# Kernel tuning notes

Hardware: AMD Instinct MI355X
Metric: run time of the kernel (lower is better)

The kernel has to match this reference:

```python
import jax, jax.numpy as jnp
import numpy as np

N = 100000       # nodes
E = 1600000      # edges (avg degree 16)
IN_DIM = 128
HIDDEN = 128


def _glorot(key, shape):
    s = 1.0 / np.sqrt(shape[0])
    return jax.random.uniform(key, shape, minval=-s, maxval=s, dtype=jnp.float32)


def setup_inputs() -> dict:
    key = jax.random.key(0)
    ks = jax.random.split(key, 8)
    x = jax.random.normal(ks[0], (N, IN_DIM), dtype=jnp.float32)
    edge_index = jax.random.randint(ks[1], (2, E), 0, N, dtype=jnp.int32)
    W0 = _glorot(ks[2], (IN_DIM, HIDDEN))
    b0 = jnp.zeros((HIDDEN,), dtype=jnp.float32)
    W1 = _glorot(ks[3], (HIDDEN, HIDDEN))
    b1 = jnp.zeros((HIDDEN,), dtype=jnp.float32)
    W2 = _glorot(ks[4], (HIDDEN, HIDDEN))
    b2 = jnp.zeros((HIDDEN,), dtype=jnp.float32)
    return {"x": x, "edge_index": edge_index,
            "W0": W0, "b0": b0, "W1": W1, "b1": b1, "W2": W2, "b2": b2}


def _gcn_conv(x, row, col, norm, W, b):
    # x' = W x, then out[i] = sum_{j in N(i) U {i}} norm_ji * x'[j], + bias
    h = x @ W                              # [N, out]
    msg = norm[:, None] * h[row]           # [E+N, out] gather + scale
    out = jax.ops.segment_sum(msg, col, num_segments=N)  # scatter-add
    return out + b


def reference(x, edge_index, W0, b0, W1, b1, W2, b2):
    # PyG GCNConv default: add self-loops, symmetric normalization D^-1/2 A D^-1/2
    self_loops = jnp.arange(N, dtype=edge_index.dtype)
    row = jnp.concatenate([edge_index[0], self_loops])  # sources
    col = jnp.concatenate([edge_index[1], self_loops])  # destinations
    deg = jax.ops.segment_sum(jnp.ones_like(col, dtype=x.dtype), col, num_segments=N)
    dinv = jax.lax.rsqrt(deg)              # deg >= 1 thanks to self-loops
    norm = dinv[row] * dinv[col]           # [E+N]

    h = _gcn_conv(x, row, col, norm, W0, b0)
    h = jax.nn.relu(h)                     # dropout: eval mode (identity)
    h = _gcn_conv(h, row, col, norm, W1, b1)
    h = jax.nn.relu(h)
    return _gcn_conv(h, row, col, norm, W2, b2)
```

## Files before the change

### kernel.cpp

```cpp
#include <hip/hip_runtime.h>

#define HID 128
#define BR  128
#define FILL_CHUNK 2048

typedef _Float16 f16;
typedef f16 f16x2 __attribute__((ext_vector_type(2)));
typedef f16 f16x4 __attribute__((ext_vector_type(4)));
typedef f16 f16x8 __attribute__((ext_vector_type(8)));
typedef float f32x4 __attribute__((ext_vector_type(4)));

static __device__ __forceinline__ float2 h2f(unsigned int u) {
    f16x2 v;
    __builtin_memcpy(&v, &u, 4);
    return make_float2((float)v[0], (float)v[1]);
}


__global__ void k_deg_count(const int* __restrict__ col, int* __restrict__ cnt, int E) {
    int e = blockIdx.x * 256 + threadIdx.x;
    if (e < E) atomicAdd(&cnt[col[e]], 1);
}

__global__ void k_scan_block(const int* __restrict__ cnt, int* __restrict__ excl,
                             int* __restrict__ bsum, float* __restrict__ dinv, int N) {
    __shared__ int s[256];
    int i = blockIdx.x * 256 + threadIdx.x;
    int v = (i < N) ? cnt[i] : 0;
    if (i < N) dinv[i] = 1.0f / sqrtf((float)(v + 1));
    s[threadIdx.x] = v;
    __syncthreads();
    for (int off = 1; off < 256; off <<= 1) {
        int t = (threadIdx.x >= off) ? s[threadIdx.x - off] : 0;
        __syncthreads();
        s[threadIdx.x] += t;
        __syncthreads();
    }
    if (i < N) excl[i] = s[threadIdx.x] - v;
    if (threadIdx.x == 255) bsum[blockIdx.x] = s[255];
}

__global__ __launch_bounds__(1024) void k_scan_bsum(int* __restrict__ bsum, int nb) {
    __shared__ int s[1024];
    int i = threadIdx.x;
    int v = (i < nb) ? bsum[i] : 0;
    s[i] = v;
    __syncthreads();
    for (int off = 1; off < 1024; off <<= 1) {
        int t = (i >= off) ? s[i - off] : 0;
        __syncthreads();
        s[i] += t;
        __syncthreads();
    }
    if (i < nb) bsum[i] = s[i] - v;
}

__global__ void k_scan_add(int* __restrict__ row_ptr, const int* __restrict__ bsum,
                           int* __restrict__ fill, int N, int E) {
    int i = blockIdx.x * 256 + threadIdx.x;
    if (i < N) {
        int v = row_ptr[i] + bsum[blockIdx.x];
        row_ptr[i] = v;
        fill[i] = v;
    }
    if (i == 0) row_ptr[N] = E;
}

__global__ void k_fill(const int* __restrict__ row, const int* __restrict__ col,
                       int* __restrict__ fill, int* __restrict__ csr_src, int E, int N) {
    const int xcd = blockIdx.x & 7;
    const int chunk = blockIdx.x >> 3;
    const int per = (N + 7) >> 3;
    const int lo = xcd * per;
    const int hi = min(N, lo + per);
    const int eend = min(E, (chunk + 1) * FILL_CHUNK);
    for (int e = chunk * FILL_CHUNK + threadIdx.x; e < eend; e += 256) {
        int c = col[e];
        if (c >= lo && c < hi) {
            int p = atomicAdd(&fill[c], 1);
            csr_src[p] = row[e];
        }
    }
}


__global__ void k_wprep(const float* __restrict__ W, f16* __restrict__ out) {
    int i = blockIdx.x * 256 + threadIdx.x;
    if (i >= 4096) return;
    int k = i >> 5, n0 = (i & 31) * 4;
    float4 v = reinterpret_cast<const float4*>(W)[i];
    float vv[4] = {v.x, v.y, v.z, v.w};
#pragma unroll
    for (int e = 0; e < 4; ++e) {
        int n = n0 + e;
        int idx = (k >> 3) * 1024 + n * 8 + (k & 7);
        f16 h = (f16)vv[e];
        out[idx] = h;
        out[16384 + idx] = (f16)(vv[e] - (float)h);
    }
}


__global__ __launch_bounds__(512, 4) void k_gemm(const float* __restrict__ X,
                                                 const f16* __restrict__ Wt,
                                                 const float* __restrict__ dinv,
                                                 f16* __restrict__ H,
                                                 int N, int relu_in) {
    __shared__ f16 Xs[2 * 16384];
    const int t = threadIdx.x;
    const int row0 = blockIdx.x * BR;

    const int w  = t >> 6;
    const int l  = t & 63;
    const int lg = l >> 4;
    const int li = l & 15;
    const int rg = w >> 2;
    const int cg = w & 3;

    f16x8 Bh[2][4], Bl[2][4];
#pragma unroll
    for (int cb = 0; cb < 2; ++cb) {
        const int ncol = cg * 32 + cb * 16 + li;
#pragma unroll
        for (int ks = 0; ks < 4; ++ks) {
            const int idx = (ks * 4 + lg) * 1024 + ncol * 8;
            Bh[cb][ks] = *reinterpret_cast<const f16x8*>(&Wt[idx]);
            Bl[cb][ks] = *reinterpret_cast<const f16x8*>(&Wt[16384 + idx]);
        }
    }

    for (int i = t; i < 4096; i += 512) {
        int r = i >> 5, q = i & 31;
        int gr = row0 + r;
        float4 v = make_float4(0.f, 0.f, 0.f, 0.f);
        if (gr < N) {
            v = reinterpret_cast<const float4*>(X + (size_t)gr * HID)[q];
            if (relu_in) {
                v.x = fmaxf(v.x, 0.f); v.y = fmaxf(v.y, 0.f);
                v.z = fmaxf(v.z, 0.f); v.w = fmaxf(v.w, 0.f);
            }
        }
        f16 h0 = (f16)v.x, h1 = (f16)v.y, h2 = (f16)v.z, h3 = (f16)v.w;
        f16 l0 = (f16)(v.x - (float)h0), l1 = (f16)(v.y - (float)h1);
        f16 l2 = (f16)(v.z - (float)h2), l3 = (f16)(v.w - (float)h3);
        int base = r * 128 + (((q >> 1) ^ (r & 7)) * 8) + (q & 1) * 4;
        *reinterpret_cast<f16x4*>(&Xs[base])         = (f16x4){h0, h1, h2, h3};
        *reinterpret_cast<f16x4*>(&Xs[16384 + base]) = (f16x4){l0, l1, l2, l3};
    }
    __syncthreads();

    f32x4 acc[4][2];
#pragma unroll
    for (int rb = 0; rb < 4; ++rb)
#pragma unroll
        for (int cb = 0; cb < 2; ++cb) acc[rb][cb] = (f32x4){0.f, 0.f, 0.f, 0.f};

#pragma unroll
    for (int rb = 0; rb < 4; ++rb) {
        const int arow = rg * 64 + rb * 16 + li;
#pragma unroll
        for (int ks = 0; ks < 4; ++ks) {
            const int idx = arow * 128 + (((ks * 4 + lg) ^ (arow & 7)) * 8);
            f16x8 Ah = *reinterpret_cast<const f16x8*>(&Xs[idx]);
            f16x8 Al = *reinterpret_cast<const f16x8*>(&Xs[16384 + idx]);
#pragma unroll
            for (int cb = 0; cb < 2; ++cb) {
                acc[rb][cb] = __builtin_amdgcn_mfma_f32_16x16x32_f16(Ah, Bh[cb][ks], acc[rb][cb], 0, 0, 0);
                acc[rb][cb] = __builtin_amdgcn_mfma_f32_16x16x32_f16(Ah, Bl[cb][ks], acc[rb][cb], 0, 0, 0);
                acc[rb][cb] = __builtin_amdgcn_mfma_f32_16x16x32_f16(Al, Bh[cb][ks], acc[rb][cb], 0, 0, 0);
            }
        }
    }

#pragma unroll
    for (int rb = 0; rb < 4; ++rb) {
#pragma unroll
        for (int r = 0; r < 4; ++r) {
            const int grow = row0 + rg * 64 + rb * 16 + lg * 4 + r;
            if (grow < N) {
                const float d = dinv[grow];
#pragma unroll
                for (int cb = 0; cb < 2; ++cb)
                    H[(size_t)grow * HID + cg * 32 + cb * 16 + li] = (f16)(acc[rb][cb][r] * d);
            }
        }
    }
}


__global__ __launch_bounds__(256) void k_agg_csr(const f16* __restrict__ h,
                                                 const int* __restrict__ csr_src,
                                                 const int* __restrict__ row_ptr,
                                                 const float* __restrict__ dinv,
                                                 const float* __restrict__ bias,
                                                 float* __restrict__ out, int N) {
    int node = (blockIdx.x * 256 + threadIdx.x) >> 6;
    if (node >= N) return;
    int lane = threadIdx.x & 63;
    const unsigned int* h32 = reinterpret_cast<const unsigned int*>(h);

    float2 self = h2f(h32[(size_t)node * 64 + lane]);
    float accx = self.x, accy = self.y;

    int j = row_ptr[node];
    const int end = row_ptr[node + 1];

    for (; j + 8 <= end; j += 8) {
        int s0 = csr_src[j];
        int s1 = csr_src[j + 1];
        int s2 = csr_src[j + 2];
        int s3 = csr_src[j + 3];
        int s4 = csr_src[j + 4];
        int s5 = csr_src[j + 5];
        int s6 = csr_src[j + 6];
        int s7 = csr_src[j + 7];
        unsigned int u0 = h32[(size_t)s0 * 64 + lane];
        unsigned int u1 = h32[(size_t)s1 * 64 + lane];
        unsigned int u2 = h32[(size_t)s2 * 64 + lane];
        unsigned int u3 = h32[(size_t)s3 * 64 + lane];
        unsigned int u4 = h32[(size_t)s4 * 64 + lane];
        unsigned int u5 = h32[(size_t)s5 * 64 + lane];
        unsigned int u6 = h32[(size_t)s6 * 64 + lane];
        unsigned int u7 = h32[(size_t)s7 * 64 + lane];
        float2 v0 = h2f(u0), v1 = h2f(u1), v2 = h2f(u2), v3 = h2f(u3);
        float2 v4 = h2f(u4), v5 = h2f(u5), v6 = h2f(u6), v7 = h2f(u7);
        accx += ((v0.x + v1.x) + (v2.x + v3.x)) + ((v4.x + v5.x) + (v6.x + v7.x));
        accy += ((v0.y + v1.y) + (v2.y + v3.y)) + ((v4.y + v5.y) + (v6.y + v7.y));
    }
    for (; j < end; ++j) {
        float2 v = h2f(h32[(size_t)csr_src[j] * 64 + lane]);
        accx += v.x;
        accy += v.y;
    }

    float di = dinv[node];
    int c = lane * 2;
    float2 o;
    o.x = fmaf(di, accx, bias[c]);
    o.y = fmaf(di, accy, bias[c + 1]);
    *reinterpret_cast<float2*>(out + (size_t)node * HID + c) = o;
}


extern "C" void kernel_launch(void* const* d_in, const int* in_sizes, int n_in,
                              void* d_out, int out_size, void* d_ws, size_t ws_size,
                              hipStream_t stream) {
    const float* x  = (const float*)d_in[0];
    const int*   ei = (const int*)  d_in[1];
    const float* W0 = (const float*)d_in[2];
    const float* b0 = (const float*)d_in[3];
    const float* W1 = (const float*)d_in[4];
    const float* b1 = (const float*)d_in[5];
    const float* W2 = (const float*)d_in[6];
    const float* b2 = (const float*)d_in[7];

    const int N = in_sizes[0] / HID;
    const int E = in_sizes[1] / 2;
    const int* row = ei;
    const int* col = ei + E;

    const int nb_n = (N + 255) / 256;

    f16*   h16     = (f16*)d_ws;
    float* dinv    = (float*)(h16 + (size_t)N * HID);
    int*   cnt     = (int*)(dinv + N);
    int*   row_ptr = cnt + N;
    int*   fill    = row_ptr + (N + 1);
    int*   bsum    = fill + N;
    int*   csr_src = bsum + nb_n;
    f16*   wt0     = (f16*)(csr_src + E);
    f16*   wt1     = wt0 + 32768;
    f16*   wt2     = wt1 + 32768;
    float* out     = (float*)d_out;

    const int nb_e    = (E + 255) / 256;
    const int nb_gemm = (N + BR - 1) / BR;
    const int nb_agg  = (N * 64 + 255) / 256;
    const int nb_fill = ((E + FILL_CHUNK - 1) / FILL_CHUNK) * 8;

    hipMemsetAsync(cnt, 0, (size_t)N * sizeof(int), stream);
    k_wprep<<<16, 256, 0, stream>>>(W0, wt0);
    k_wprep<<<16, 256, 0, stream>>>(W1, wt1);
    k_wprep<<<16, 256, 0, stream>>>(W2, wt2);
    k_deg_count <<<nb_e, 256, 0, stream>>>(col, cnt, E);
    k_scan_block<<<nb_n, 256, 0, stream>>>(cnt, row_ptr, bsum, dinv, N);
    k_scan_bsum <<<1, 1024, 0, stream>>>(bsum, nb_n);
    k_scan_add  <<<nb_n, 256, 0, stream>>>(row_ptr, bsum, fill, N, E);
    k_fill      <<<nb_fill, 256, 0, stream>>>(row, col, fill, csr_src, E, N);

    k_gemm   <<<nb_gemm, 512, 0, stream>>>(x, wt0, dinv, h16, N, 0);
    k_agg_csr<<<nb_agg, 256, 0, stream>>>(h16, csr_src, row_ptr, dinv, b0, out, N);
    k_gemm   <<<nb_gemm, 512, 0, stream>>>(out, wt1, dinv, h16, N, 1);
    k_agg_csr<<<nb_agg, 256, 0, stream>>>(h16, csr_src, row_ptr, dinv, b1, out, N);
    k_gemm   <<<nb_gemm, 512, 0, stream>>>(out, wt2, dinv, h16, N, 1);
    k_agg_csr<<<nb_agg, 256, 0, stream>>>(h16, csr_src, row_ptr, dinv, b2, out, N);
}
```

Baseline: 471.2 us.

## Split aggregation columns into 8 slices across blocks, 8 lanes per node

The CSR aggregation kernel now assigns each node to 8 threads covering a 16-column slice, with the column slice picked by blockIdx modulo 8, so a block handles 32 nodes over one slice. Consecutive blocks sweep the same nodes' neighbours across column slices, which aims to improve L2 locality for gathered rows and raise node-level parallelism per wave. Index loads and output stores become nontemporal, and the unroll drops from 8 to 4. Each gather is now only a 32-byte segment per node, which may reduce coalescing efficiency and repeats the csr_src reads eight times.

New measurement: 940.8 us. 2x slower.

```diff
diff --git a/kernel.cpp b/kernel.cpp
--- a/kernel.cpp
+++ b/kernel.cpp
@@ -194,51 +194,43 @@
                                                  const float* __restrict__ dinv,
                                                  const float* __restrict__ bias,
                                                  float* __restrict__ out, int N) {
-    int node = (blockIdx.x * 256 + threadIdx.x) >> 6;
+    const int g    = blockIdx.x & 7;
+    const int node = (blockIdx.x >> 3) * 32 + (threadIdx.x >> 3);
     if (node >= N) return;
-    int lane = threadIdx.x & 63;
+    const int r    = threadIdx.x & 7;
+    const int colu = g * 8 + r;
     const unsigned int* h32 = reinterpret_cast<const unsigned int*>(h);
 
-    float2 self = h2f(h32[(size_t)node * 64 + lane]);
+    float2 self = h2f(h32[(size_t)node * 64 + colu]);
     float accx = self.x, accy = self.y;
 
     int j = row_ptr[node];
     const int end = row_ptr[node + 1];
 
-    for (; j + 8 <= end; j += 8) {
-        int s0 = csr_src[j];
-        int s1 = csr_src[j + 1];
-        int s2 = csr_src[j + 2];
-        int s3 = csr_src[j + 3];
-        int s4 = csr_src[j + 4];
-        int s5 = csr_src[j + 5];
-        int s6 = csr_src[j + 6];
-        int s7 = csr_src[j + 7];
-        unsigned int u0 = h32[(size_t)s0 * 64 + lane];
-        unsigned int u1 = h32[(size_t)s1 * 64 + lane];
-        unsigned int u2 = h32[(size_t)s2 * 64 + lane];
-        unsigned int u3 = h32[(size_t)s3 * 64 + lane];
-        unsigned int u4 = h32[(size_t)s4 * 64 + lane];
-        unsigned int u5 = h32[(size_t)s5 * 64 + lane];
-        unsigned int u6 = h32[(size_t)s6 * 64 + lane];
-        unsigned int u7 = h32[(size_t)s7 * 64 + lane];
+    for (; j + 4 <= end; j += 4) {
+        int s0 = __builtin_nontemporal_load(csr_src + j);
+        int s1 = __builtin_nontemporal_load(csr_src + j + 1);
+        int s2 = __builtin_nontemporal_load(csr_src + j + 2);
+        int s3 = __builtin_nontemporal_load(csr_src + j + 3);
+        unsigned int u0 = h32[(size_t)s0 * 64 + colu];
+        unsigned int u1 = h32[(size_t)s1 * 64 + colu];
+        unsigned int u2 = h32[(size_t)s2 * 64 + colu];
+        unsigned int u3 = h32[(size_t)s3 * 64 + colu];
         float2 v0 = h2f(u0), v1 = h2f(u1), v2 = h2f(u2), v3 = h2f(u3);
-        float2 v4 = h2f(u4), v5 = h2f(u5), v6 = h2f(u6), v7 = h2f(u7);
-        accx += ((v0.x + v1.x) + (v2.x + v3.x)) + ((v4.x + v5.x) + (v6.x + v7.x));
-        accy += ((v0.y + v1.y) + (v2.y + v3.y)) + ((v4.y + v5.y) + (v6.y + v7.y));
+        accx += (v0.x + v1.x) + (v2.x + v3.x);
+        accy += (v0.y + v1.y) + (v2.y + v3.y);
     }
     for (; j < end; ++j) {
-        float2 v = h2f(h32[(size_t)csr_src[j] * 64 + lane]);
+        int s = __builtin_nontemporal_load(csr_src + j);
+        float2 v = h2f(h32[(size_t)s * 64 + colu]);
         accx += v.x;
         accy += v.y;
     }
 
-    float di = dinv[node];
-    int c = lane * 2;
-    float2 o;
-    o.x = fmaf(di, accx, bias[c]);
-    o.y = fmaf(di, accy, bias[c + 1]);
-    *reinterpret_cast<float2*>(out + (size_t)node * HID + c) = o;
+    const float di = dinv[node];
+    const int c = colu * 2;
+    __builtin_nontemporal_store(fmaf(di, accx, bias[c]),     out + (size_t)node * HID + c);
+    __builtin_nontemporal_store(fmaf(di, accy, bias[c + 1]), out + (size_t)node * HID + c + 1);
 }
 
 
@@ -275,7 +267,7 @@
 
     const int nb_e    = (E + 255) / 256;
     const int nb_gemm = (N + BR - 1) / BR;
-    const int nb_agg  = (N * 64 + 255) / 256;
+    const int nb_agg  = ((N + 31) / 32) * 8;
     const int nb_fill = ((E + FILL_CHUNK - 1) / FILL_CHUNK) * 8;
 
     hipMemsetAsync(cnt, 0, (size_t)N * sizeof(int), stream);
```
